# Kernel optimization log

Measured on AMD Instinct MI355X. Metric: run time of the kernel, lower is better.

Reference implementation:

```python
import jax, jax.numpy as jnp
import numpy as np
import math

D_MODEL = 1024
D_STATE = 128
EXPAND = 2
HEADDIM = 64
NGROUPS = 1
ROPE_FRACTION = 0.5
A_FLOOR = 1e-4
D_INNER = EXPAND * D_MODEL            # 2048
NHEADS = D_INNER // HEADDIM           # 32
SPLIT = int(D_STATE * ROPE_FRACTION)  # 64
R = SPLIT // 2                        # 32 rotary angles; rotary applied to first R state dims
D_IN_PROJ = 2 * D_INNER + 2 * D_STATE * NGROUPS + 3 * NHEADS + R  # 4480
BATCH = 1
SEQLEN = 1024


def setup_inputs() -> dict:
    key = jax.random.key(0)
    k0, k1, k2, k3 = jax.random.split(key, 4)
    u = jax.random.normal(k0, (BATCH, SEQLEN, D_MODEL), jnp.float32)
    w_in = jax.random.normal(k1, (D_IN_PROJ, D_MODEL), jnp.float32) * (D_MODEL ** -0.5)
    w_out = jax.random.normal(k2, (D_MODEL, D_INNER), jnp.float32) * (D_INNER ** -0.5)
    # dt_bias init matches torch: inverse-softplus of dt ~ LogUniform(dt_min, dt_max)
    dt = jnp.exp(jax.random.uniform(k3, (NHEADS,), jnp.float32)
                 * (math.log(0.1) - math.log(0.001)) + math.log(0.001))
    dt = jnp.maximum(dt, 1e-4)
    dt_bias = dt + jnp.log(-jnp.expm1(-dt))
    D = jnp.ones((NHEADS,), jnp.float32)
    return {"u": u, "w_in": w_in, "w_out": w_out, "dt_bias": dt_bias, "D": D}


def _mamba3_forward(u, w_in, w_out, dt_bias, D):
    b, l, _ = u.shape
    proj = u @ w_in.T  # [b, l, D_IN_PROJ]
    sizes = [D_INNER, D_INNER, D_STATE * NGROUPS, D_STATE * NGROUPS, NHEADS, NHEADS, NHEADS, R]
    idx = np.cumsum(sizes)[:-1]
    z, x, B, C, dd_dt, dd_A, trap, angles = jnp.split(proj, idx, axis=-1)

    A = jnp.minimum(-jax.nn.softplus(dd_A), -A_FLOOR)      # [b,l,h]
    dt = jax.nn.softplus(dd_dt + dt_bias)                  # [b,l,h]
    tr = jax.nn.sigmoid(trap)                              # [b,l,h]
    # rotary angle: tanh(angles)[b,l,1,R] * dt[b,l,h,1] * pi, cumsum over time
    theta = jnp.cumsum(jnp.tanh(angles)[:, :, None, :] * dt[..., None] * jnp.pi, axis=1)  # [b,l,h,R]

    x_h = x.reshape(b, l, NHEADS, HEADDIM)
    z_h = z.reshape(b, l, NHEADS, HEADDIM)
    B_h = B.reshape(b, l, NGROUPS, D_STATE)[:, :, 0, :]  # only group 0 is read in the loop
    C_h = C.reshape(b, l, NGROUPS, D_STATE)[:, :, 0, :]

    def step(carry, inp):
        sr, si, px = carry  # sr: [b,h,p,n], si: [b,h,p,R] (imag beyond R is identically zero)
        dt_t, A_t, tr_t, th, bt, ct, xt = inp
        alpha = jnp.exp(A_t * dt_t)[:, :, None, None]          # [b,h,1,1]
        beta = ((1.0 - tr_t) * dt_t)[:, :, None, None] * alpha
        gamma = (tr_t * dt_t)[:, :, None, None]
        base = bt[:, None, None, :] * (px[..., None] * beta + xt[..., None] * gamma)  # [b,h,p,n]
        rc = jnp.cos(th)[:, :, None, :]  # [b,h,1,R]
        rs = jnp.sin(th)[:, :, None, :]
        sr = sr * alpha + jnp.concatenate([base[..., :R] * rc, base[..., R:]], axis=-1)
        si = si * alpha + base[..., :R] * rs
        ctb = ct[:, None, None, :]
        y = (jnp.sum((sr[..., :R] * rc + si * rs) * ctb[..., :R], axis=-1)
             + jnp.sum(sr[..., R:] * ctb[..., R:], axis=-1))  # [b,h,p]
        return (sr, si, xt), y

    sr0 = jnp.zeros((b, NHEADS, HEADDIM, D_STATE), u.dtype)
    si0 = jnp.zeros((b, NHEADS, HEADDIM, R), u.dtype)
    px0 = jnp.zeros((b, NHEADS, HEADDIM), u.dtype)
    xs = (jnp.moveaxis(dt, 1, 0), jnp.moveaxis(A, 1, 0), jnp.moveaxis(tr, 1, 0),
          jnp.moveaxis(theta, 1, 0), jnp.moveaxis(B_h, 1, 0), jnp.moveaxis(C_h, 1, 0),
          jnp.moveaxis(x_h, 1, 0))
    _, ys = jax.lax.scan(step, (sr0, si0, px0), xs)  # [l,b,h,p]
    y = jnp.moveaxis(ys, 0, 1) + D[None, None, :, None] * x_h
    out = y * jax.nn.silu(z_h)
    return out.reshape(b, l, D_INNER) @ w_out.T


def reference(u, w_in, w_out, dt_bias, D):
    return _mamba3_forward(u, w_in, w_out, dt_bias, D)
```

## Files before the change

kernel.cpp:

```cpp
#include <hip/hip_runtime.h>
#include <math.h>

#define L_SEQ   1024
#define DMODEL  1024
#define DINNER  2048
#define NH      32
#define HD      64
#define NS      160
#define RR      32
#define NPROJ   4480
#define OFF_Z   0
#define OFF_X   2048
#define OFF_B   4096
#define OFF_C   4224
#define OFF_DT  4352
#define OFF_A   4384
#define OFF_TR  4416
#define OFF_ANG 4448
#define NC      16
#define CL      64
#define PIF     3.14159265358979323846f

typedef __attribute__((ext_vector_type(8))) short bf16x8;
typedef __attribute__((ext_vector_type(4))) float f32x4;
typedef unsigned int u32;
typedef unsigned short u16;

__device__ __forceinline__ float softplusf(float x) {
  return (x > 20.f) ? x : log1pf(expf(x));
}
__device__ __forceinline__ u16 f2bf(float f) {
  u32 u = __float_as_uint(f);
  u32 r = (u + 0x7FFFu + ((u >> 16) & 1u)) >> 16;
  return (u16)r;
}
__device__ __forceinline__ float bf2f(u16 v) {
  return __uint_as_float(((u32)v) << 16);
}

__device__ __forceinline__ void gload_lds16(const u16* g, u16* l) {
  __builtin_amdgcn_global_load_lds(
      (const __attribute__((address_space(1))) u32*)(unsigned long long)(const void*)g,
      (__attribute__((address_space(3))) u32*)(unsigned long long)(void*)l, 16, 0, 0);
}

__global__ __launch_bounds__(256) void cvt2_bf16(
    const float* __restrict__ s0, u16* __restrict__ d0, int q0,
    const float* __restrict__ s1, u16* __restrict__ d1, int q1) {
  int i = blockIdx.x * 256 + threadIdx.x;
  const float* s; u16* d; int j;
  if (i < q0) { s = s0; d = d0; j = i; }
  else { j = i - q0; if (j >= q1) return; s = s1; d = d1; }
  const float4* s4 = (const float4*)s;
  float4 a = s4[2 * j], b = s4[2 * j + 1];
  union { u16 h[8]; uint4 v; } o;
  o.h[0] = f2bf(a.x); o.h[1] = f2bf(a.y); o.h[2] = f2bf(a.z); o.h[3] = f2bf(a.w);
  o.h[4] = f2bf(b.x); o.h[5] = f2bf(b.y); o.h[6] = f2bf(b.z); o.h[7] = f2bf(b.w);
  ((uint4*)d)[j] = o.v;
}

template <int BM, int BN, int NBM, int TOT>
__global__ __launch_bounds__(256) void gemm_bf16(
    const u16* __restrict__ A, const u16* __restrict__ B,
    float* __restrict__ C, int N, int K) {
  constexpr int BK = 32;
  constexpr int WM = BM / 2, WN = BN / 2;
  constexpr int MF = WM / 16, NF = WN / 16;
  constexpr int CA = BM / 64;
  constexpr int CB = BN / 64;
  __shared__ u16 lds[(BM + BN) * BK];

  const int i = blockIdx.x;
  const int j = (i & 7) * (TOT / 8) + (i >> 3);
  const int bm = (j % NBM) * BM;
  const int bn = (j / NBM) * BN;

  const int tid = threadIdx.x, w = tid >> 6, lane = tid & 63;
  const int wr = w >> 1, wc = w & 1;
  const int fr = lane & 15, sl = lane >> 4;
  const int lrow = lane >> 2, lslot = (lane & 3) * 8;

  const u16* gA[CA]; u16* lA[CA];
#pragma unroll
  for (int jj = 0; jj < CA; ++jj) {
    int ca = w * CA + jj;
    gA[jj] = A + (size_t)(bm + ca * 16 + lrow) * K + lslot;
    lA[jj] = lds + ca * 512;
  }
  const u16* gB[CB]; u16* lB[CB];
#pragma unroll
  for (int jj = 0; jj < CB; ++jj) {
    int cb = w * CB + jj;
    gB[jj] = B + (size_t)(bn + cb * 16 + lrow) * K + lslot;
    lB[jj] = lds + BM * 32 + cb * 512;
  }

  const u16* aptr[MF]; const u16* bptr[NF];
#pragma unroll
  for (int ii = 0; ii < MF; ++ii)
    aptr[ii] = lds + (wr * WM + ii * 16 + fr) * 32 + sl * 8;
#pragma unroll
  for (int jj = 0; jj < NF; ++jj)
    bptr[jj] = lds + BM * 32 + (wc * WN + jj * 16 + fr) * 32 + sl * 8;

  f32x4 acc[MF][NF] = {};
  const int iters = K / BK;

#pragma unroll
  for (int jj = 0; jj < CA; ++jj) gload_lds16(gA[jj], lA[jj]);
#pragma unroll
  for (int jj = 0; jj < CB; ++jj) gload_lds16(gB[jj], lB[jj]);

  for (int it = 0; it < iters; ++it) {
    __syncthreads();
    bf16x8 af[MF], bfv[NF];
#pragma unroll
    for (int ii = 0; ii < MF; ++ii) af[ii] = *(const bf16x8*)aptr[ii];
#pragma unroll
    for (int jj = 0; jj < NF; ++jj) bfv[jj] = *(const bf16x8*)bptr[jj];
    __syncthreads();
    if (it + 1 < iters) {
#pragma unroll
      for (int jj = 0; jj < CA; ++jj) gload_lds16(gA[jj] + (it + 1) * BK, lA[jj]);
#pragma unroll
      for (int jj = 0; jj < CB; ++jj) gload_lds16(gB[jj] + (it + 1) * BK, lB[jj]);
    }
#pragma unroll
    for (int ii = 0; ii < MF; ++ii)
#pragma unroll
      for (int jj = 0; jj < NF; ++jj)
        acc[ii][jj] = __builtin_amdgcn_mfma_f32_16x16x32_bf16(
            af[ii], bfv[jj], acc[ii][jj], 0, 0, 0);
  }

#pragma unroll
  for (int ii = 0; ii < MF; ++ii) {
    int rb = bm + wr * WM + ii * 16 + sl * 4;
#pragma unroll
    for (int jj = 0; jj < NF; ++jj) {
      int cb = bn + wc * WN + jj * 16 + fr;
#pragma unroll
      for (int r = 0; r < 4; ++r)
        C[(size_t)(rb + r) * N + cb] = acc[ii][jj][r];
    }
  }
}

__global__ __launch_bounds__(256) void prep_scalars_cvt(
    const float* __restrict__ proj, const float* __restrict__ dt_bias,
    float* __restrict__ dtA, float* __restrict__ lnaA,
    float* __restrict__ betaA, float* __restrict__ gammaA,
    float* __restrict__ angP,
    const float* __restrict__ wsrc, u16* __restrict__ wdst) {
  const int b = blockIdx.x;
  if (b < 1024) {
    int j = b * 256 + threadIdx.x;
    const float4* s4 = (const float4*)wsrc;
    float4 a = s4[2 * j], bb = s4[2 * j + 1];
    union { u16 h[8]; uint4 v; } o;
    o.h[0] = f2bf(a.x); o.h[1] = f2bf(a.y); o.h[2] = f2bf(a.z); o.h[3] = f2bf(a.w);
    o.h[4] = f2bf(bb.x); o.h[5] = f2bf(bb.y); o.h[6] = f2bf(bb.z); o.h[7] = f2bf(bb.w);
    ((uint4*)wdst)[j] = o.v;
    return;
  }
  int idx = (b - 1024) * 256 + threadIdx.x;
  int h = idx & 31, l = idx >> 5;
  const float* prow = proj + (size_t)l * NPROJ;
  float dt = softplusf(prow[OFF_DT + h] + dt_bias[h]);
  float Apos = fmaxf(softplusf(prow[OFF_A + h]), 1e-4f);
  float tr = 1.f / (1.f + expf(-prow[OFF_TR + h]));
  float lna = -Apos * dt;
  float alpha = expf(lna);
  dtA[idx] = dt;
  lnaA[idx] = lna;
  betaA[idx] = (1.f - tr) * dt * alpha;
  gammaA[idx] = tr * dt;
  angP[idx] = tanhf(prow[OFF_ANG + h]) * PIF;
}

__global__ __launch_bounds__(256) void theta_scan(
    const float* __restrict__ angP, const float* __restrict__ dtA,
    float* __restrict__ rc, float* __restrict__ rs) {
  const int h = blockIdx.x >> 5;
  const int r = blockIdx.x & 31;
  const int tid = threadIdx.x;
  __shared__ float ldssc[256];

  float csum[4];
  float run = 0.f;
#pragma unroll
  for (int i = 0; i < 4; ++i) {
    int l = tid * 4 + i;
    run += angP[l * NH + r] * dtA[l * NH + h];
    csum[i] = run;
  }
  ldssc[tid] = run;
  __syncthreads();
  for (int off = 1; off < 256; off <<= 1) {
    float t = (tid >= off) ? ldssc[tid - off] : 0.f;
    __syncthreads();
    ldssc[tid] += t;
    __syncthreads();
  }
  float excl = ldssc[tid] - run;
#pragma unroll
  for (int i = 0; i < 4; ++i) {
    int l = tid * 4 + i;
    float th = excl + csum[i];
    size_t o = ((size_t)l * NH + h) * RR + r;
    rc[o] = cosf(th);
    rs[o] = sinf(th);
  }
}

__global__ __launch_bounds__(256) void uvgA(
    const float* __restrict__ proj, const float* __restrict__ betaA,
    const float* __restrict__ gammaA, const float* __restrict__ lnaA,
    const float* __restrict__ rc, const float* __restrict__ rs,
    u16* __restrict__ U, u16* __restrict__ V, u16* __restrict__ Gt,
    float* __restrict__ cumA, float* __restrict__ adec,
    u16* __restrict__ S) {
  const int h = blockIdx.x >> 4, c = blockIdx.x & 15;
  const int c0 = c * CL;
  const int tid = threadIdx.x;
  const int w = tid >> 6, lane = tid & 63;

  __shared__ __attribute__((aligned(16))) char smem[54784];
  u16 (*Gw)[72]   = (u16(*)[72])(smem);
  float* wsc      = (float*)(smem + 9216);
  float* bet      = (float*)(smem + 9472);
  float* gam      = (float*)(smem + 9728);
  float (*xs)[64] = (float(*)[64])(smem + 10240);
  u16 (*Vl)[168]  = (u16(*)[168])(smem + 10240);
  u16 (*Vt)[72]   = (u16(*)[72])(smem + 31744);

  if (w < 3) {
    for (int i = tid; i < 65 * 16; i += 192) {
      int r = i >> 4, c4 = i & 15;
      int l = c0 - 1 + r;
      float4 v = {0.f, 0.f, 0.f, 0.f};
      if (l >= 0)
        v = *(const float4*)(proj + (size_t)l * NPROJ + OFF_X + h * HD + c4 * 4);
      *(float4*)&xs[r][c4 * 4] = v;
    }
  } else {
    const int t = lane;
    float v = lnaA[(c0 + t) * NH + h];
#pragma unroll
    for (int k = 1; k < 64; k <<= 1) {
      int src = t - k;
      float o = __shfl(v, src < 0 ? 0 : src);
      if (t >= k) v += o;
    }
    cumA[(size_t)h * L_SEQ + c0 + t] = v;
    if (t == 63) adec[h * NC + c] = expf(v);
    float c63 = __shfl(v, 63);
    wsc[t] = expf(c63 - v);
    bet[t] = betaA[(c0 + t) * NH + h];
    gam[t] = gammaA[(c0 + t) * NH + h];
  }
  __syncthreads();

  {
    const int p = lane;
    union { u16 hh[16]; uint4 q[2]; } og, ow;
    float xprev = xs[w * 16][p];
#pragma unroll
    for (int i = 0; i < 16; ++i) {
      int s = w * 16 + i;
      float xcur = xs[s + 1][p];
      float g = bet[s] * xprev + gam[s] * xcur;
      og.hh[i] = f2bf(g);
      ow.hh[i] = f2bf(g * wsc[s]);
      xprev = xcur;
    }
    uint4* gdst = (uint4*)(Gt + (((size_t)h * NC + c) * HD + p) * CL + w * 16);
    gdst[0] = og.q[0];
    gdst[1] = og.q[1];
    *(uint4*)&Gw[p][w * 16] = ow.q[0];
    *(uint4*)&Gw[p][w * 16 + 8] = ow.q[1];
  }
  __syncthreads();

  if (tid < 160) {
    const int n = tid;
    const int idxB = (n < 64) ? (n & 31) : (n - 32);
    const bool is_re = (n < 32);
    const bool has_rot = (n < 64);
    for (int ss = 0; ss < 64; ++ss) {
      int l = c0 + ss;
      const float* prow = proj + (size_t)l * NPROJ;
      float Bv = prow[OFF_B + idxB];
      float Cv = prow[OFF_C + idxB];
      if (has_rot) {
        float rv = is_re ? rc[((size_t)l * NH + h) * RR + idxB]
                         : rs[((size_t)l * NH + h) * RR + idxB];
        Bv *= rv; Cv *= rv;
      }
      u16 bb = f2bf(Bv);
      U[((size_t)h * L_SEQ + l) * NS + n] = f2bf(Cv);
      V[((size_t)h * L_SEQ + l) * NS + n] = bb;
      Vl[ss][n] = bb;
    }
  }
  __syncthreads();

  if (tid < 160) {
    int n = tid;
#pragma unroll
    for (int s2 = 0; s2 < 32; ++s2) {
      u32 lo = Vl[2 * s2][n], hi = Vl[2 * s2 + 1][n];
      *(u32*)&Vt[n][2 * s2] = lo | (hi << 16);
    }
  }
  __syncthreads();

  const int wr = w >> 1, wc = w & 1;
  const int fr = lane & 15, sl = lane >> 4;
  f32x4 acc[2][5] = {};
#pragma unroll
  for (int ks = 0; ks < 2; ++ks) {
    bf16x8 a0 = *(const bf16x8*)&Gw[wr * 32 + fr][ks * 32 + sl * 8];
    bf16x8 a1 = *(const bf16x8*)&Gw[wr * 32 + 16 + fr][ks * 32 + sl * 8];
    bf16x8 bv[5];
#pragma unroll
    for (int fj = 0; fj < 5; ++fj)
      bv[fj] = *(const bf16x8*)&Vt[wc * 80 + fj * 16 + fr][ks * 32 + sl * 8];
#pragma unroll
    for (int fj = 0; fj < 5; ++fj) {
      acc[0][fj] = __builtin_amdgcn_mfma_f32_16x16x32_bf16(a0, bv[fj], acc[0][fj], 0, 0, 0);
      acc[1][fj] = __builtin_amdgcn_mfma_f32_16x16x32_bf16(a1, bv[fj], acc[1][fj], 0, 0, 0);
    }
  }
  u16* Fb = S + (size_t)(c * NH + h) * HD * NS;
#pragma unroll
  for (int fi = 0; fi < 2; ++fi)
#pragma unroll
    for (int fj = 0; fj < 5; ++fj)
#pragma unroll
      for (int r = 0; r < 4; ++r) {
        int p = wr * 32 + fi * 16 + sl * 4 + r;
        int n = wc * 80 + fj * 16 + fr;
        Fb[(size_t)p * NS + n] = f2bf(acc[fi][fj][r]);
      }
}

__global__ __launch_bounds__(256) void combine(
    u16* __restrict__ S, const float* __restrict__ adec) {
  const int idx = blockIdx.x * 256 + threadIdx.x;
  if (idx >= NH * HD * NS) return;
  const int n = idx % NS;
  const int rem = idx / NS;
  const int p = rem & 63;
  const int h = rem >> 6;
  float F = 0.f;
  for (int c = 0; c < NC; ++c) {
    size_t off = ((size_t)(c * NH + h) * HD + p) * NS + n;
    float sv = bf2f(S[off]);
    S[off] = f2bf(F);
    F = fmaf(F, adec[h * NC + c], sv);
  }
}

__global__ __launch_bounds__(256) void passB(
    const float* __restrict__ proj, const u16* __restrict__ U,
    const u16* __restrict__ V, const u16* __restrict__ Gt,
    const float* __restrict__ cumA, const u16* __restrict__ S,
    const float* __restrict__ Dvec, u16* __restrict__ yz) {
  const int c = blockIdx.x >> 5, h = blockIdx.x & 31;
  const int c0 = c * CL;
  const int tid = threadIdx.x;
  const int w = tid >> 6, lane = tid & 63;
  const int wr = w >> 1, wc = w & 1;
  const int fr = lane & 15, sl = lane >> 4;
  __shared__ u16 Ul[64][168];
  __shared__ u16 BB[64][168];
  __shared__ u16 Ml[64][72];
  __shared__ u16 Gl[64][72];
  __shared__ float cums[64], ecum[64];

  const u16* Us = U + ((size_t)h * L_SEQ + c0) * NS;
  for (int i = tid; i < 1280; i += 256) {
    int r = i / 20, ch = i % 20;
    *(uint4*)&Ul[r][ch * 8] = *(const uint4*)(Us + (size_t)r * NS + ch * 8);
  }
  {
    const u16* S0 = S + (size_t)(c * NH + h) * HD * NS;
    for (int i = tid; i < 1280; i += 256) {
      int r = i / 20, ch = i % 20;
      *(uint4*)&BB[r][ch * 8] = *(const uint4*)(S0 + (size_t)r * NS + ch * 8);
    }
  }
  if (tid < 64) {
    float cv = cumA[(size_t)h * L_SEQ + c0 + tid];
    cums[tid] = cv;
    ecum[tid] = expf(cv);
  }
  __syncthreads();

  f32x4 acc[2][2] = {};
#pragma unroll
  for (int ks = 0; ks < 5; ++ks) {
    bf16x8 a0 = *(const bf16x8*)&Ul[wr * 32 + fr][ks * 32 + sl * 8];
    bf16x8 a1 = *(const bf16x8*)&Ul[wr * 32 + 16 + fr][ks * 32 + sl * 8];
    bf16x8 b0 = *(const bf16x8*)&BB[wc * 32 + fr][ks * 32 + sl * 8];
    bf16x8 b1 = *(const bf16x8*)&BB[wc * 32 + 16 + fr][ks * 32 + sl * 8];
    acc[0][0] = __builtin_amdgcn_mfma_f32_16x16x32_bf16(a0, b0, acc[0][0], 0, 0, 0);
    acc[0][1] = __builtin_amdgcn_mfma_f32_16x16x32_bf16(a0, b1, acc[0][1], 0, 0, 0);
    acc[1][0] = __builtin_amdgcn_mfma_f32_16x16x32_bf16(a1, b0, acc[1][0], 0, 0, 0);
    acc[1][1] = __builtin_amdgcn_mfma_f32_16x16x32_bf16(a1, b1, acc[1][1], 0, 0, 0);
  }
#pragma unroll
  for (int fi = 0; fi < 2; ++fi)
#pragma unroll
    for (int fj = 0; fj < 2; ++fj)
#pragma unroll
      for (int r = 0; r < 4; ++r)
        acc[fi][fj][r] *= ecum[wr * 32 + fi * 16 + sl * 4 + r];
  __syncthreads();

  const u16* Vs = V + ((size_t)h * L_SEQ + c0) * NS;
  for (int i = tid; i < 1280; i += 256) {
    int r = i / 20, ch = i % 20;
    *(uint4*)&BB[r][ch * 8] = *(const uint4*)(Vs + (size_t)r * NS + ch * 8);
  }
  const u16* Gs = Gt + ((size_t)h * NC + c) * HD * CL;
  for (int i = tid; i < 512; i += 256) {
    int p = i >> 3, ch = i & 7;
    *(uint4*)&Gl[p][ch * 8] = *(const uint4*)(Gs + (size_t)p * CL + ch * 8);
  }
  __syncthreads();

  f32x4 pac[2][2] = {};
#pragma unroll
  for (int ks = 0; ks < 5; ++ks) {
    bf16x8 a0 = *(const bf16x8*)&Ul[wr * 32 + fr][ks * 32 + sl * 8];
    bf16x8 a1 = *(const bf16x8*)&Ul[wr * 32 + 16 + fr][ks * 32 + sl * 8];
    bf16x8 b0 = *(const bf16x8*)&BB[wc * 32 + fr][ks * 32 + sl * 8];
    bf16x8 b1 = *(const bf16x8*)&BB[wc * 32 + 16 + fr][ks * 32 + sl * 8];
    pac[0][0] = __builtin_amdgcn_mfma_f32_16x16x32_bf16(a0, b0, pac[0][0], 0, 0, 0);
    pac[0][1] = __builtin_amdgcn_mfma_f32_16x16x32_bf16(a0, b1, pac[0][1], 0, 0, 0);
    pac[1][0] = __builtin_amdgcn_mfma_f32_16x16x32_bf16(a1, b0, pac[1][0], 0, 0, 0);
    pac[1][1] = __builtin_amdgcn_mfma_f32_16x16x32_bf16(a1, b1, pac[1][1], 0, 0, 0);
  }
#pragma unroll
  for (int fi = 0; fi < 2; ++fi)
#pragma unroll
    for (int fj = 0; fj < 2; ++fj)
#pragma unroll
      for (int r = 0; r < 4; ++r) {
        int t = wr * 32 + fi * 16 + sl * 4 + r;
        int ss = wc * 32 + fj * 16 + fr;
        float m = (ss <= t) ? expf(cums[t] - cums[ss]) * pac[fi][fj][r] : 0.f;
        Ml[t][ss] = f2bf(m);
      }
  __syncthreads();

#pragma unroll
  for (int ks = 0; ks < 2; ++ks) {
    bf16x8 a0 = *(const bf16x8*)&Ml[wr * 32 + fr][ks * 32 + sl * 8];
    bf16x8 a1 = *(const bf16x8*)&Ml[wr * 32 + 16 + fr][ks * 32 + sl * 8];
    bf16x8 b0 = *(const bf16x8*)&Gl[wc * 32 + fr][ks * 32 + sl * 8];
    bf16x8 b1 = *(const bf16x8*)&Gl[wc * 32 + 16 + fr][ks * 32 + sl * 8];
    acc[0][0] = __builtin_amdgcn_mfma_f32_16x16x32_bf16(a0, b0, acc[0][0], 0, 0, 0);
    acc[0][1] = __builtin_amdgcn_mfma_f32_16x16x32_bf16(a0, b1, acc[0][1], 0, 0, 0);
    acc[1][0] = __builtin_amdgcn_mfma_f32_16x16x32_bf16(a1, b0, acc[1][0], 0, 0, 0);
    acc[1][1] = __builtin_amdgcn_mfma_f32_16x16x32_bf16(a1, b1, acc[1][1], 0, 0, 0);
  }

  const float Dh = Dvec[h];
#pragma unroll
  for (int fi = 0; fi < 2; ++fi)
#pragma unroll
    for (int fj = 0; fj < 2; ++fj)
#pragma unroll
      for (int r = 0; r < 4; ++r) {
        int t = wr * 32 + fi * 16 + sl * 4 + r;
        int p = wc * 32 + fj * 16 + fr;
        int l = c0 + t;
        float x = proj[(size_t)l * NPROJ + OFF_X + h * HD + p];
        float z = proj[(size_t)l * NPROJ + OFF_Z + h * HD + p];
        float y = acc[fi][fj][r] + Dh * x;
        float sg = z / (1.f + expf(-z));
        yz[(size_t)l * DINNER + h * HD + p] = f2bf(y * sg);
      }
}

extern "C" void kernel_launch(void* const* d_in, const int* in_sizes, int n_in,
                              void* d_out, int out_size, void* d_ws, size_t ws_size,
                              hipStream_t stream) {
  const float* u       = (const float*)d_in[0];
  const float* w_in    = (const float*)d_in[1];
  const float* w_out   = (const float*)d_in[2];
  const float* dt_bias = (const float*)d_in[3];
  const float* Dvec    = (const float*)d_in[4];
  float* out = (float*)d_out;

  float* ws = (float*)d_ws;
  float* proj   = ws;
  float* dtA    = proj + 4587520;
  float* lnaA   = dtA + 32768;
  float* betaA  = lnaA + 32768;
  float* gammaA = betaA + 32768;
  float* cumA   = gammaA + 32768;
  float* adec   = cumA + 32768;
  float* angP   = adec + 512;
  float* rcb    = angP + 32768;
  float* rsb    = rcb + 1048576;
  u16*   Sb     = (u16*)(rsb + 1048576);
  u16*   Gtb    = Sb + 5242880;
  u16*   Ubuf   = Gtb + 2097152;
  u16*   Vbuf   = Ubuf + 5242880;
  u16*   yzb    = Vbuf + 5242880;
  u16*   wob    = yzb + 2097152;
  u16*   ub     = Sb;
  u16*   wib    = Sb + 1048576;

  cvt2_bf16<<<(131072 + 573440) / 256, 256, 0, stream>>>(
      u, ub, 131072, w_in, wib, 573440);

  gemm_bf16<64, 128, 16, 560><<<560, 256, 0, stream>>>(
      ub, wib, proj, NPROJ, DMODEL);

  prep_scalars_cvt<<<1024 + 128, 256, 0, stream>>>(
      proj, dt_bias, dtA, lnaA, betaA, gammaA, angP, w_out, wob);

  theta_scan<<<NH * RR, 256, 0, stream>>>(angP, dtA, rcb, rsb);

  uvgA<<<NH * NC, 256, 0, stream>>>(
      proj, betaA, gammaA, lnaA, rcb, rsb, Ubuf, Vbuf, Gtb, cumA, adec, Sb);

  combine<<<(NH * HD * NS + 255) / 256, 256, 0, stream>>>(Sb, adec);

  passB<<<NC * NH, 256, 0, stream>>>(
      proj, Ubuf, Vbuf, Gtb, cumA, Sb, Dvec, yzb);

  gemm_bf16<64, 64, 16, 256><<<256, 256, 0, stream>>>(
      yzb, wob, out, DMODEL, DINNER);
}
```

Measured before the change: 131.2 us.

## Fuse theta scan into prep kernel and fold chunk-state combine into passB

Merges the theta cumulative-sum kernel into the scalar prep/weight-convert kernel, recomputing tanh and softplus directly from proj instead of staging dt and angle buffers. Removes the separate combine kernel: each passB block now rebuilds its incoming chunk state by a decayed sum over all earlier chunk states while loading into shared memory. This drops two launches and intermediate buffer traffic, but passB now does redundant, serial work that grows with chunk index (up to 15 extra state reads per element), which adds load imbalance and rounds the state to bf16 only once at the end.

```diff
diff --git a/kernel.cpp b/kernel.cpp
--- a/kernel.cpp
+++ b/kernel.cpp
@@ -146,15 +146,18 @@
   }
 }
 
-__global__ __launch_bounds__(256) void prep_scalars_cvt(
+__global__ __launch_bounds__(256) void prep_theta_cvt(
     const float* __restrict__ proj, const float* __restrict__ dt_bias,
-    float* __restrict__ dtA, float* __restrict__ lnaA,
-    float* __restrict__ betaA, float* __restrict__ gammaA,
-    float* __restrict__ angP,
+    float* __restrict__ lnaA, float* __restrict__ betaA,
+    float* __restrict__ gammaA, float* __restrict__ rc,
+    float* __restrict__ rs,
     const float* __restrict__ wsrc, u16* __restrict__ wdst) {
   const int b = blockIdx.x;
+  const int tid = threadIdx.x;
+  __shared__ float ldssc[256];
+
   if (b < 1024) {
-    int j = b * 256 + threadIdx.x;
+    int j = b * 256 + tid;
     const float4* s4 = (const float4*)wsrc;
     float4 a = s4[2 * j], bb = s4[2 * j + 1];
     union { u16 h[8]; uint4 v; } o;
@@ -163,35 +166,33 @@
     ((uint4*)wdst)[j] = o.v;
     return;
   }
-  int idx = (b - 1024) * 256 + threadIdx.x;
-  int h = idx & 31, l = idx >> 5;
-  const float* prow = proj + (size_t)l * NPROJ;
-  float dt = softplusf(prow[OFF_DT + h] + dt_bias[h]);
-  float Apos = fmaxf(softplusf(prow[OFF_A + h]), 1e-4f);
-  float tr = 1.f / (1.f + expf(-prow[OFF_TR + h]));
-  float lna = -Apos * dt;
-  float alpha = expf(lna);
-  dtA[idx] = dt;
-  lnaA[idx] = lna;
-  betaA[idx] = (1.f - tr) * dt * alpha;
-  gammaA[idx] = tr * dt;
-  angP[idx] = tanhf(prow[OFF_ANG + h]) * PIF;
-}
-
-__global__ __launch_bounds__(256) void theta_scan(
-    const float* __restrict__ angP, const float* __restrict__ dtA,
-    float* __restrict__ rc, float* __restrict__ rs) {
-  const int h = blockIdx.x >> 5;
-  const int r = blockIdx.x & 31;
-  const int tid = threadIdx.x;
-  __shared__ float ldssc[256];
+  if (b < 1152) {
+    int idx = (b - 1024) * 256 + tid;
+    int h = idx & 31, l = idx >> 5;
+    const float* prow = proj + (size_t)l * NPROJ;
+    float dt = softplusf(prow[OFF_DT + h] + dt_bias[h]);
+    float Apos = fmaxf(softplusf(prow[OFF_A + h]), 1e-4f);
+    float tr = 1.f / (1.f + expf(-prow[OFF_TR + h]));
+    float lna = -Apos * dt;
+    float alpha = expf(lna);
+    lnaA[idx] = lna;
+    betaA[idx] = (1.f - tr) * dt * alpha;
+    gammaA[idx] = tr * dt;
+    return;
+  }
+  const int ch = b - 1152;
+  const int h = ch >> 5;
+  const int r = ch & 31;
 
   float csum[4];
   float run = 0.f;
 #pragma unroll
   for (int i = 0; i < 4; ++i) {
     int l = tid * 4 + i;
-    run += angP[l * NH + r] * dtA[l * NH + h];
+    const float* prow = proj + (size_t)l * NPROJ;
+    float ap = tanhf(prow[OFF_ANG + r]) * PIF;
+    float dtv = softplusf(prow[OFF_DT + h] + dt_bias[h]);
+    run += ap * dtv;
     csum[i] = run;
   }
   ldssc[tid] = run;
@@ -345,28 +346,12 @@
       }
 }
 
-__global__ __launch_bounds__(256) void combine(
-    u16* __restrict__ S, const float* __restrict__ adec) {
-  const int idx = blockIdx.x * 256 + threadIdx.x;
-  if (idx >= NH * HD * NS) return;
-  const int n = idx % NS;
-  const int rem = idx / NS;
-  const int p = rem & 63;
-  const int h = rem >> 6;
-  float F = 0.f;
-  for (int c = 0; c < NC; ++c) {
-    size_t off = ((size_t)(c * NH + h) * HD + p) * NS + n;
-    float sv = bf2f(S[off]);
-    S[off] = f2bf(F);
-    F = fmaf(F, adec[h * NC + c], sv);
-  }
-}
-
 __global__ __launch_bounds__(256) void passB(
     const float* __restrict__ proj, const u16* __restrict__ U,
     const u16* __restrict__ V, const u16* __restrict__ Gt,
-    const float* __restrict__ cumA, const u16* __restrict__ S,
-    const float* __restrict__ Dvec, u16* __restrict__ yz) {
+    const float* __restrict__ cumA, const u16* __restrict__ Fin,
+    const float* __restrict__ adec, const float* __restrict__ Dvec,
+    u16* __restrict__ yz) {
   const int c = blockIdx.x >> 5, h = blockIdx.x & 31;
   const int c0 = c * CL;
   const int tid = threadIdx.x;
@@ -377,24 +362,44 @@
   __shared__ u16 BB[64][168];
   __shared__ u16 Ml[64][72];
   __shared__ u16 Gl[64][72];
-  __shared__ float cums[64], ecum[64];
+  __shared__ float cums[64], ecum[64], ad[16];
 
   const u16* Us = U + ((size_t)h * L_SEQ + c0) * NS;
   for (int i = tid; i < 1280; i += 256) {
     int r = i / 20, ch = i % 20;
     *(uint4*)&Ul[r][ch * 8] = *(const uint4*)(Us + (size_t)r * NS + ch * 8);
   }
-  {
-    const u16* S0 = S + (size_t)(c * NH + h) * HD * NS;
-    for (int i = tid; i < 1280; i += 256) {
-      int r = i / 20, ch = i % 20;
-      *(uint4*)&BB[r][ch * 8] = *(const uint4*)(S0 + (size_t)r * NS + ch * 8);
-    }
-  }
   if (tid < 64) {
     float cv = cumA[(size_t)h * L_SEQ + c0 + tid];
     cums[tid] = cv;
     ecum[tid] = expf(cv);
+  } else if (tid < 80) {
+    ad[tid - 64] = adec[h * NC + (tid - 64)];
+  }
+  __syncthreads();
+
+  for (int i = tid; i < 1280; i += 256) {
+    int r = i / 20, ch = i % 20;
+    float a0 = 0.f, a1 = 0.f, a2 = 0.f, a3 = 0.f,
+          a4 = 0.f, a5 = 0.f, a6 = 0.f, a7 = 0.f;
+    for (int cp = 0; cp < c; ++cp) {
+      float av = ad[cp];
+      uint4 v = *(const uint4*)(Fin + (size_t)(cp * NH + h) * HD * NS +
+                                (size_t)r * NS + ch * 8);
+      const u16* hh = (const u16*)&v;
+      a0 = fmaf(a0, av, bf2f(hh[0]));
+      a1 = fmaf(a1, av, bf2f(hh[1]));
+      a2 = fmaf(a2, av, bf2f(hh[2]));
+      a3 = fmaf(a3, av, bf2f(hh[3]));
+      a4 = fmaf(a4, av, bf2f(hh[4]));
+      a5 = fmaf(a5, av, bf2f(hh[5]));
+      a6 = fmaf(a6, av, bf2f(hh[6]));
+      a7 = fmaf(a7, av, bf2f(hh[7]));
+    }
+    union { u16 hh[8]; uint4 v; } o;
+    o.hh[0] = f2bf(a0); o.hh[1] = f2bf(a1); o.hh[2] = f2bf(a2); o.hh[3] = f2bf(a3);
+    o.hh[4] = f2bf(a4); o.hh[5] = f2bf(a5); o.hh[6] = f2bf(a6); o.hh[7] = f2bf(a7);
+    *(uint4*)&BB[r][ch * 8] = o.v;
   }
   __syncthreads();
 
@@ -498,14 +503,12 @@
 
   float* ws = (float*)d_ws;
   float* proj   = ws;
-  float* dtA    = proj + 4587520;
-  float* lnaA   = dtA + 32768;
+  float* lnaA   = proj + 4587520;
   float* betaA  = lnaA + 32768;
   float* gammaA = betaA + 32768;
   float* cumA   = gammaA + 32768;
   float* adec   = cumA + 32768;
-  float* angP   = adec + 512;
-  float* rcb    = angP + 32768;
+  float* rcb    = adec + 512;
   float* rsb    = rcb + 1048576;
   u16*   Sb     = (u16*)(rsb + 1048576);
   u16*   Gtb    = Sb + 5242880;
@@ -522,18 +525,14 @@
   gemm_bf16<64, 128, 16, 560><<<560, 256, 0, stream>>>(
       ub, wib, proj, NPROJ, DMODEL);
 
-  prep_scalars_cvt<<<1024 + 128, 256, 0, stream>>>(
-      proj, dt_bias, dtA, lnaA, betaA, gammaA, angP, w_out, wob);
-
-  theta_scan<<<NH * RR, 256, 0, stream>>>(angP, dtA, rcb, rsb);
+  prep_theta_cvt<<<1024 + 128 + 1024, 256, 0, stream>>>(
+      proj, dt_bias, lnaA, betaA, gammaA, rcb, rsb, w_out, wob);
 
   uvgA<<<NH * NC, 256, 0, stream>>>(
       proj, betaA, gammaA, lnaA, rcb, rsb, Ubuf, Vbuf, Gtb, cumA, adec, Sb);
 
-  combine<<<(NH * HD * NS + 255) / 256, 256, 0, stream>>>(Sb, adec);
-
   passB<<<NC * NH, 256, 0, stream>>>(
-      proj, Ubuf, Vbuf, Gtb, cumA, Sb, Dvec, yzb);
+      proj, Ubuf, Vbuf, Gtb, cumA, Sb, adec, Dvec, yzb);
 
   gemm_bf16<64, 64, 16, 256><<<256, 256, 0, stream>>>(
       yzb, wob, out, DMODEL, DINNER);
```

New measurement: 135.6 us. +3.4%, slower.

## Move intra-chunk diagonal output into the chunk-state kernel, dropping V/G buffers

Applied to the files above, without the earlier changes.

The intra-chunk (diagonal) part of the chunked SSM output, C·Bᵀ masked by decay and multiplied by the G input, is now computed in uvgA while the chunk's B, C and G are already in shared memory. It is written out as a bf16 partial Y. The final pass then only adds the inter-chunk state contribution scaled by exp(cumA) plus the skip and gate terms. This removes the global writes and re-reads of the V and Gt buffers and shortens the final kernel. In exchange uvgA needs more shared memory (about 76KB), which may lower occupancy, and the partial Y is rounded to bf16 before it is summed.

```diff
diff --git a/kernel.cpp b/kernel.cpp
--- a/kernel.cpp
+++ b/kernel.cpp
@@ -217,22 +217,26 @@
     const float* __restrict__ proj, const float* __restrict__ betaA,
     const float* __restrict__ gammaA, const float* __restrict__ lnaA,
     const float* __restrict__ rc, const float* __restrict__ rs,
-    u16* __restrict__ U, u16* __restrict__ V, u16* __restrict__ Gt,
-    float* __restrict__ cumA, float* __restrict__ adec,
-    u16* __restrict__ S) {
+    u16* __restrict__ U, float* __restrict__ cumA, float* __restrict__ adec,
+    u16* __restrict__ S, u16* __restrict__ Yb) {
   const int h = blockIdx.x >> 4, c = blockIdx.x & 15;
   const int c0 = c * CL;
   const int tid = threadIdx.x;
   const int w = tid >> 6, lane = tid & 63;
-
-  __shared__ __attribute__((aligned(16))) char smem[54784];
-  u16 (*Gw)[72]   = (u16(*)[72])(smem);
+  const int wr = w >> 1, wc = w & 1;
+  const int fr = lane & 15, sl = lane >> 4;
+
+  __shared__ __attribute__((aligned(16))) char smem[76288];
+  u16 (*Gl)[72]   = (u16(*)[72])(smem);
   float* wsc      = (float*)(smem + 9216);
   float* bet      = (float*)(smem + 9472);
   float* gam      = (float*)(smem + 9728);
+  float* cums     = (float*)(smem + 9984);
   float (*xs)[64] = (float(*)[64])(smem + 10240);
-  u16 (*Vl)[168]  = (u16(*)[168])(smem + 10240);
-  u16 (*Vt)[72]   = (u16(*)[72])(smem + 31744);
+  u16 (*Ul)[168]  = (u16(*)[168])(smem + 10240);
+  u16 (*Vl)[168]  = (u16(*)[168])(smem + 31744);
+  u16 (*Vt)[72]   = (u16(*)[72])(smem + 53248);
+  u16 (*Ml)[72]   = (u16(*)[72])(smem + 53248);
 
   if (w < 3) {
     for (int i = tid; i < 65 * 16; i += 192) {
@@ -255,6 +259,7 @@
     cumA[(size_t)h * L_SEQ + c0 + t] = v;
     if (t == 63) adec[h * NC + c] = expf(v);
     float c63 = __shfl(v, 63);
+    cums[t] = v;
     wsc[t] = expf(c63 - v);
     bet[t] = betaA[(c0 + t) * NH + h];
     gam[t] = gammaA[(c0 + t) * NH + h];
@@ -263,22 +268,17 @@
 
   {
     const int p = lane;
-    union { u16 hh[16]; uint4 q[2]; } og, ow;
+    union { u16 hh[16]; uint4 q[2]; } og;
     float xprev = xs[w * 16][p];
 #pragma unroll
     for (int i = 0; i < 16; ++i) {
       int s = w * 16 + i;
       float xcur = xs[s + 1][p];
-      float g = bet[s] * xprev + gam[s] * xcur;
-      og.hh[i] = f2bf(g);
-      ow.hh[i] = f2bf(g * wsc[s]);
+      og.hh[i] = f2bf(bet[s] * xprev + gam[s] * xcur);
       xprev = xcur;
     }
-    uint4* gdst = (uint4*)(Gt + (((size_t)h * NC + c) * HD + p) * CL + w * 16);
-    gdst[0] = og.q[0];
-    gdst[1] = og.q[1];
-    *(uint4*)&Gw[p][w * 16] = ow.q[0];
-    *(uint4*)&Gw[p][w * 16 + 8] = ow.q[1];
+    *(uint4*)&Gl[p][w * 16] = og.q[0];
+    *(uint4*)&Gl[p][w * 16 + 8] = og.q[1];
   }
   __syncthreads();
 
@@ -297,10 +297,10 @@
                          : rs[((size_t)l * NH + h) * RR + idxB];
         Bv *= rv; Cv *= rv;
       }
-      u16 bb = f2bf(Bv);
-      U[((size_t)h * L_SEQ + l) * NS + n] = f2bf(Cv);
-      V[((size_t)h * L_SEQ + l) * NS + n] = bb;
-      Vl[ss][n] = bb;
+      u16 uu = f2bf(Cv);
+      U[((size_t)h * L_SEQ + l) * NS + n] = uu;
+      Ul[ss][n] = uu;
+      Vl[ss][n] = f2bf(Bv);
     }
   }
   __syncthreads();
@@ -309,40 +309,93 @@
     int n = tid;
 #pragma unroll
     for (int s2 = 0; s2 < 32; ++s2) {
-      u32 lo = Vl[2 * s2][n], hi = Vl[2 * s2 + 1][n];
+      float w0 = wsc[2 * s2], w1 = wsc[2 * s2 + 1];
+      u32 lo = (u32)f2bf(bf2f(Vl[2 * s2][n]) * w0);
+      u32 hi = (u32)f2bf(bf2f(Vl[2 * s2 + 1][n]) * w1);
       *(u32*)&Vt[n][2 * s2] = lo | (hi << 16);
     }
   }
   __syncthreads();
 
-  const int wr = w >> 1, wc = w & 1;
-  const int fr = lane & 15, sl = lane >> 4;
-  f32x4 acc[2][5] = {};
-#pragma unroll
-  for (int ks = 0; ks < 2; ++ks) {
-    bf16x8 a0 = *(const bf16x8*)&Gw[wr * 32 + fr][ks * 32 + sl * 8];
-    bf16x8 a1 = *(const bf16x8*)&Gw[wr * 32 + 16 + fr][ks * 32 + sl * 8];
-    bf16x8 bv[5];
-#pragma unroll
-    for (int fj = 0; fj < 5; ++fj)
-      bv[fj] = *(const bf16x8*)&Vt[wc * 80 + fj * 16 + fr][ks * 32 + sl * 8];
-#pragma unroll
-    for (int fj = 0; fj < 5; ++fj) {
-      acc[0][fj] = __builtin_amdgcn_mfma_f32_16x16x32_bf16(a0, bv[fj], acc[0][fj], 0, 0, 0);
-      acc[1][fj] = __builtin_amdgcn_mfma_f32_16x16x32_bf16(a1, bv[fj], acc[1][fj], 0, 0, 0);
-    }
-  }
-  u16* Fb = S + (size_t)(c * NH + h) * HD * NS;
+  {
+    f32x4 acc[2][5] = {};
+#pragma unroll
+    for (int ks = 0; ks < 2; ++ks) {
+      bf16x8 a0 = *(const bf16x8*)&Gl[wr * 32 + fr][ks * 32 + sl * 8];
+      bf16x8 a1 = *(const bf16x8*)&Gl[wr * 32 + 16 + fr][ks * 32 + sl * 8];
+      bf16x8 bv[5];
+#pragma unroll
+      for (int fj = 0; fj < 5; ++fj)
+        bv[fj] = *(const bf16x8*)&Vt[wc * 80 + fj * 16 + fr][ks * 32 + sl * 8];
+#pragma unroll
+      for (int fj = 0; fj < 5; ++fj) {
+        acc[0][fj] = __builtin_amdgcn_mfma_f32_16x16x32_bf16(a0, bv[fj], acc[0][fj], 0, 0, 0);
+        acc[1][fj] = __builtin_amdgcn_mfma_f32_16x16x32_bf16(a1, bv[fj], acc[1][fj], 0, 0, 0);
+      }
+    }
+    u16* Fb = S + (size_t)(c * NH + h) * HD * NS;
+#pragma unroll
+    for (int fi = 0; fi < 2; ++fi)
+#pragma unroll
+      for (int fj = 0; fj < 5; ++fj)
+#pragma unroll
+        for (int r = 0; r < 4; ++r) {
+          int p = wr * 32 + fi * 16 + sl * 4 + r;
+          int n = wc * 80 + fj * 16 + fr;
+          Fb[(size_t)p * NS + n] = f2bf(acc[fi][fj][r]);
+        }
+  }
+
+  f32x4 pac[2][2] = {};
+#pragma unroll
+  for (int ks = 0; ks < 5; ++ks) {
+    bf16x8 a0 = *(const bf16x8*)&Ul[wr * 32 + fr][ks * 32 + sl * 8];
+    bf16x8 a1 = *(const bf16x8*)&Ul[wr * 32 + 16 + fr][ks * 32 + sl * 8];
+    bf16x8 b0 = *(const bf16x8*)&Vl[wc * 32 + fr][ks * 32 + sl * 8];
+    bf16x8 b1 = *(const bf16x8*)&Vl[wc * 32 + 16 + fr][ks * 32 + sl * 8];
+    pac[0][0] = __builtin_amdgcn_mfma_f32_16x16x32_bf16(a0, b0, pac[0][0], 0, 0, 0);
+    pac[0][1] = __builtin_amdgcn_mfma_f32_16x16x32_bf16(a0, b1, pac[0][1], 0, 0, 0);
+    pac[1][0] = __builtin_amdgcn_mfma_f32_16x16x32_bf16(a1, b0, pac[1][0], 0, 0, 0);
+    pac[1][1] = __builtin_amdgcn_mfma_f32_16x16x32_bf16(a1, b1, pac[1][1], 0, 0, 0);
+  }
+  __syncthreads();
 #pragma unroll
   for (int fi = 0; fi < 2; ++fi)
 #pragma unroll
-    for (int fj = 0; fj < 5; ++fj)
+    for (int fj = 0; fj < 2; ++fj)
 #pragma unroll
       for (int r = 0; r < 4; ++r) {
-        int p = wr * 32 + fi * 16 + sl * 4 + r;
-        int n = wc * 80 + fj * 16 + fr;
-        Fb[(size_t)p * NS + n] = f2bf(acc[fi][fj][r]);
+        int t = wr * 32 + fi * 16 + sl * 4 + r;
+        int ss = wc * 32 + fj * 16 + fr;
+        float m = (ss <= t) ? expf(cums[t] - cums[ss]) * pac[fi][fj][r] : 0.f;
+        Ml[t][ss] = f2bf(m);
       }
+  __syncthreads();
+
+  {
+    f32x4 yac[2][2] = {};
+#pragma unroll
+    for (int ks = 0; ks < 2; ++ks) {
+      bf16x8 a0 = *(const bf16x8*)&Ml[wr * 32 + fr][ks * 32 + sl * 8];
+      bf16x8 a1 = *(const bf16x8*)&Ml[wr * 32 + 16 + fr][ks * 32 + sl * 8];
+      bf16x8 b0 = *(const bf16x8*)&Gl[wc * 32 + fr][ks * 32 + sl * 8];
+      bf16x8 b1 = *(const bf16x8*)&Gl[wc * 32 + 16 + fr][ks * 32 + sl * 8];
+      yac[0][0] = __builtin_amdgcn_mfma_f32_16x16x32_bf16(a0, b0, yac[0][0], 0, 0, 0);
+      yac[0][1] = __builtin_amdgcn_mfma_f32_16x16x32_bf16(a0, b1, yac[0][1], 0, 0, 0);
+      yac[1][0] = __builtin_amdgcn_mfma_f32_16x16x32_bf16(a1, b0, yac[1][0], 0, 0, 0);
+      yac[1][1] = __builtin_amdgcn_mfma_f32_16x16x32_bf16(a1, b1, yac[1][1], 0, 0, 0);
+    }
+#pragma unroll
+    for (int fi = 0; fi < 2; ++fi)
+#pragma unroll
+      for (int fj = 0; fj < 2; ++fj)
+#pragma unroll
+        for (int r = 0; r < 4; ++r) {
+          int t = wr * 32 + fi * 16 + sl * 4 + r;
+          int p = wc * 32 + fj * 16 + fr;
+          Yb[(size_t)(c0 + t) * DINNER + h * HD + p] = f2bf(yac[fi][fj][r]);
+        }
+  }
 }
 
 __global__ __launch_bounds__(256) void combine(
@@ -362,11 +415,11 @@
   }
 }
 
-__global__ __launch_bounds__(256) void passB(
+__global__ __launch_bounds__(256) void passC(
     const float* __restrict__ proj, const u16* __restrict__ U,
-    const u16* __restrict__ V, const u16* __restrict__ Gt,
     const float* __restrict__ cumA, const u16* __restrict__ S,
-    const float* __restrict__ Dvec, u16* __restrict__ yz) {
+    const u16* __restrict__ Yb, const float* __restrict__ Dvec,
+    u16* __restrict__ yz) {
   const int c = blockIdx.x >> 5, h = blockIdx.x & 31;
   const int c0 = c * CL;
   const int tid = threadIdx.x;
@@ -375,9 +428,7 @@
   const int fr = lane & 15, sl = lane >> 4;
   __shared__ u16 Ul[64][168];
   __shared__ u16 BB[64][168];
-  __shared__ u16 Ml[64][72];
-  __shared__ u16 Gl[64][72];
-  __shared__ float cums[64], ecum[64];
+  __shared__ float ecum[64];
 
   const u16* Us = U + ((size_t)h * L_SEQ + c0) * NS;
   for (int i = tid; i < 1280; i += 256) {
@@ -391,11 +442,7 @@
       *(uint4*)&BB[r][ch * 8] = *(const uint4*)(S0 + (size_t)r * NS + ch * 8);
     }
   }
-  if (tid < 64) {
-    float cv = cumA[(size_t)h * L_SEQ + c0 + tid];
-    cums[tid] = cv;
-    ecum[tid] = expf(cv);
-  }
+  if (tid < 64) ecum[tid] = expf(cumA[(size_t)h * L_SEQ + c0 + tid]);
   __syncthreads();
 
   f32x4 acc[2][2] = {};
@@ -410,63 +457,6 @@
     acc[1][0] = __builtin_amdgcn_mfma_f32_16x16x32_bf16(a1, b0, acc[1][0], 0, 0, 0);
     acc[1][1] = __builtin_amdgcn_mfma_f32_16x16x32_bf16(a1, b1, acc[1][1], 0, 0, 0);
   }
-#pragma unroll
-  for (int fi = 0; fi < 2; ++fi)
-#pragma unroll
-    for (int fj = 0; fj < 2; ++fj)
-#pragma unroll
-      for (int r = 0; r < 4; ++r)
-        acc[fi][fj][r] *= ecum[wr * 32 + fi * 16 + sl * 4 + r];
-  __syncthreads();
-
-  const u16* Vs = V + ((size_t)h * L_SEQ + c0) * NS;
-  for (int i = tid; i < 1280; i += 256) {
-    int r = i / 20, ch = i % 20;
-    *(uint4*)&BB[r][ch * 8] = *(const uint4*)(Vs + (size_t)r * NS + ch * 8);
-  }
-  const u16* Gs = Gt + ((size_t)h * NC + c) * HD * CL;
-  for (int i = tid; i < 512; i += 256) {
-    int p = i >> 3, ch = i & 7;
-    *(uint4*)&Gl[p][ch * 8] = *(const uint4*)(Gs + (size_t)p * CL + ch * 8);
-  }
-  __syncthreads();
-
-  f32x4 pac[2][2] = {};
-#pragma unroll
-  for (int ks = 0; ks < 5; ++ks) {
-    bf16x8 a0 = *(const bf16x8*)&Ul[wr * 32 + fr][ks * 32 + sl * 8];
-    bf16x8 a1 = *(const bf16x8*)&Ul[wr * 32 + 16 + fr][ks * 32 + sl * 8];
-    bf16x8 b0 = *(const bf16x8*)&BB[wc * 32 + fr][ks * 32 + sl * 8];
-    bf16x8 b1 = *(const bf16x8*)&BB[wc * 32 + 16 + fr][ks * 32 + sl * 8];
-    pac[0][0] = __builtin_amdgcn_mfma_f32_16x16x32_bf16(a0, b0, pac[0][0], 0, 0, 0);
-    pac[0][1] = __builtin_amdgcn_mfma_f32_16x16x32_bf16(a0, b1, pac[0][1], 0, 0, 0);
-    pac[1][0] = __builtin_amdgcn_mfma_f32_16x16x32_bf16(a1, b0, pac[1][0], 0, 0, 0);
-    pac[1][1] = __builtin_amdgcn_mfma_f32_16x16x32_bf16(a1, b1, pac[1][1], 0, 0, 0);
-  }
-#pragma unroll
-  for (int fi = 0; fi < 2; ++fi)
-#pragma unroll
-    for (int fj = 0; fj < 2; ++fj)
-#pragma unroll
-      for (int r = 0; r < 4; ++r) {
-        int t = wr * 32 + fi * 16 + sl * 4 + r;
-        int ss = wc * 32 + fj * 16 + fr;
-        float m = (ss <= t) ? expf(cums[t] - cums[ss]) * pac[fi][fj][r] : 0.f;
-        Ml[t][ss] = f2bf(m);
-      }
-  __syncthreads();
-
-#pragma unroll
-  for (int ks = 0; ks < 2; ++ks) {
-    bf16x8 a0 = *(const bf16x8*)&Ml[wr * 32 + fr][ks * 32 + sl * 8];
-    bf16x8 a1 = *(const bf16x8*)&Ml[wr * 32 + 16 + fr][ks * 32 + sl * 8];
-    bf16x8 b0 = *(const bf16x8*)&Gl[wc * 32 + fr][ks * 32 + sl * 8];
-    bf16x8 b1 = *(const bf16x8*)&Gl[wc * 32 + 16 + fr][ks * 32 + sl * 8];
-    acc[0][0] = __builtin_amdgcn_mfma_f32_16x16x32_bf16(a0, b0, acc[0][0], 0, 0, 0);
-    acc[0][1] = __builtin_amdgcn_mfma_f32_16x16x32_bf16(a0, b1, acc[0][1], 0, 0, 0);
-    acc[1][0] = __builtin_amdgcn_mfma_f32_16x16x32_bf16(a1, b0, acc[1][0], 0, 0, 0);
-    acc[1][1] = __builtin_amdgcn_mfma_f32_16x16x32_bf16(a1, b1, acc[1][1], 0, 0, 0);
-  }
 
   const float Dh = Dvec[h];
 #pragma unroll
@@ -478,9 +468,11 @@
         int t = wr * 32 + fi * 16 + sl * 4 + r;
         int p = wc * 32 + fj * 16 + fr;
         int l = c0 + t;
+        float y = acc[fi][fj][r] * ecum[t] +
+                  bf2f(Yb[(size_t)l * DINNER + h * HD + p]);
         float x = proj[(size_t)l * NPROJ + OFF_X + h * HD + p];
         float z = proj[(size_t)l * NPROJ + OFF_Z + h * HD + p];
-        float y = acc[fi][fj][r] + Dh * x;
+        y += Dh * x;
         float sg = z / (1.f + expf(-z));
         yz[(size_t)l * DINNER + h * HD + p] = f2bf(y * sg);
       }
@@ -508,10 +500,9 @@
   float* rcb    = angP + 32768;
   float* rsb    = rcb + 1048576;
   u16*   Sb     = (u16*)(rsb + 1048576);
-  u16*   Gtb    = Sb + 5242880;
-  u16*   Ubuf   = Gtb + 2097152;
-  u16*   Vbuf   = Ubuf + 5242880;
-  u16*   yzb    = Vbuf + 5242880;
+  u16*   Ubuf   = Sb + 5242880;
+  u16*   Yb     = Ubuf + 5242880;
+  u16*   yzb    = Yb + 2097152;
   u16*   wob    = yzb + 2097152;
   u16*   ub     = Sb;
   u16*   wib    = Sb + 1048576;
@@ -528,12 +519,12 @@
   theta_scan<<<NH * RR, 256, 0, stream>>>(angP, dtA, rcb, rsb);
 
   uvgA<<<NH * NC, 256, 0, stream>>>(
-      proj, betaA, gammaA, lnaA, rcb, rsb, Ubuf, Vbuf, Gtb, cumA, adec, Sb);
+      proj, betaA, gammaA, lnaA, rcb, rsb, Ubuf, cumA, adec, Sb, Yb);
 
   combine<<<(NH * HD * NS + 255) / 256, 256, 0, stream>>>(Sb, adec);
 
-  passB<<<NC * NH, 256, 0, stream>>>(
-      proj, Ubuf, Vbuf, Gtb, cumA, Sb, Dvec, yzb);
+  passC<<<NC * NH, 256, 0, stream>>>(
+      proj, Ubuf, cumA, Sb, Yb, Dvec, yzb);
 
   gemm_bf16<64, 64, 16, 256><<<256, 256, 0, stream>>>(
       yzb, wob, out, DMODEL, DINNER);
```

After: 129.3 us. About the same (-1.4%).
